# Performance work log

Measured on AMD Instinct MI355X. Metric: run time of the kernel, lower is better.

Reference implementation:

```python
import jax, jax.numpy as jnp
import numpy as np

T, B, D_IN, UNITS = 2000, 32, 512, 1024
P_KEEP = 0.8      # eval-mode dropout mask value (1 - 0.2) for 'in', 'recur', 'orig'
BN_EPS = 1e-5     # torch BatchNorm1d default eps


def setup_inputs() -> dict:
    key = jax.random.key(0)
    ks = jax.random.split(key, 6)
    s_in = 1.0 / np.sqrt(D_IN)
    s_h = 1.0 / np.sqrt(UNITS)
    # orthogonal init for recurrent mats (as in ligru_orthinit)
    uh = jnp.linalg.qr(jax.random.normal(ks[2], (UNITS, UNITS)))[0].astype(jnp.float32)
    uz = jnp.linalg.qr(jax.random.normal(ks[3], (UNITS, UNITS)))[0].astype(jnp.float32)
    return {
        "x": jax.random.normal(ks[0], (T, B, D_IN), dtype=jnp.float32),
        "Wh": jax.random.uniform(ks[1], (UNITS, D_IN), jnp.float32, -s_in, s_in),
        "Wz": jax.random.uniform(ks[4], (UNITS, D_IN), jnp.float32, -s_in, s_in),
        "Uh": uh,
        "Uz": uz,
        "gamma_wh": jnp.ones((UNITS,), jnp.float32),
        "beta_wh": jnp.zeros((UNITS,), jnp.float32),
        "gamma_wz": jnp.ones((UNITS,), jnp.float32),
        "beta_wz": jnp.zeros((UNITS,), jnp.float32),
    }


def _batchnorm(y, gamma, beta):
    # BatchNorm1d over flattened (T*B, UNITS), biased variance (training-style stats)
    yf = y.reshape(-1, y.shape[-1])
    mean = yf.mean(axis=0)
    var = yf.var(axis=0)
    return (y - mean) * jax.lax.rsqrt(var + BN_EPS) * gamma + beta


def reference(x, Wh, Wz, Uh, Uz, gamma_wh, beta_wh, gamma_wz, beta_wz):
    # input dropout (eval mode -> constant scale 0.8) then linear, no bias (BN on)
    xd = x * P_KEEP
    wh_out = _batchnorm(jnp.einsum("tbd,ud->tbu", xd, Wh), gamma_wh, beta_wh)
    wz_out = _batchnorm(jnp.einsum("tbd,ud->tbu", xd, Wz), gamma_wz, beta_wz)

    h0 = jnp.zeros((x.shape[1], Wh.shape[0]), x.dtype)

    def step(h, inp):
        whk, wzk = inp
        z = jax.nn.sigmoid(wzk + (h * P_KEEP) @ Uz.T)   # update gate
        a = whk + (h * P_KEEP) @ Uh.T                   # candidate pre-activation
        hcand = jax.nn.relu(a) * P_KEEP                 # 'orig' dropout scale
        h_new = z * h + (1.0 - z) * hcand
        return h_new, h_new

    _, hs = jax.lax.scan(step, h0, (wh_out, wz_out))    # hs: [T, B, UNITS]
    return hs
```

## Files before the change

### kernel.cpp

```cpp
#include <hip/hip_runtime.h>


#define T_STEPS 2000
#define NCOLS   2048
#define PKEEP   0.8f
#define BN_EPSF 1e-5f

typedef __attribute__((ext_vector_type(8))) short bf16x8;
typedef __attribute__((ext_vector_type(4))) float f32x4;
typedef __attribute__((ext_vector_type(4))) unsigned int u32x4;

static __device__ __forceinline__ unsigned short f2bf(float f) {
  unsigned u = __builtin_bit_cast(unsigned, f);
  unsigned r = u + 0x7FFFu + ((u >> 16) & 1u);
  return (unsigned short)(r >> 16);
}
static __device__ __forceinline__ float bf2f(unsigned short s) {
  unsigned u = ((unsigned)s) << 16;
  return __builtin_bit_cast(float, u);
}

__global__ void k_convw(const float* __restrict__ Wh, const float* __restrict__ Wz,
                        unsigned short* __restrict__ Wb) {
  int i = blockIdx.x * 256 + threadIdx.x;
  int e = i * 4;
  int n = e >> 9;
  int k = e & 511;
  const float* src = (n < 1024) ? (Wh + (size_t)n * 512 + k)
                                : (Wz + (size_t)(n - 1024) * 512 + k);
  float4 v = *(const float4*)src;
  *(ushort4*)(Wb + e) = make_ushort4(f2bf(v.x), f2bf(v.y), f2bf(v.z), f2bf(v.w));
}

__global__ __launch_bounds__(256, 2) void k_gemm(
    const float* __restrict__ X, const unsigned short* __restrict__ Wb,
    unsigned short* __restrict__ P, float* __restrict__ sums, float* __restrict__ sumsq) {
  __shared__ __align__(16) unsigned short As[128 * 32];
  __shared__ __align__(16) unsigned short Bs[128 * 32];
  const int tid  = threadIdx.x;
  const int bm   = blockIdx.x >> 4, bn = blockIdx.x & 15;
  const int lane = tid & 63, wid = tid >> 6;
  const int wm   = wid >> 1, wn = wid & 1;
  const int lrow = lane & 15, lk = lane >> 4;

  f32x4 acc[4][4] = {};

  for (int kk = 0; kk < 512; kk += 32) {
    __syncthreads();
#pragma unroll
    for (int j = 0; j < 2; ++j) {
      int c = j * 256 + wid * 64 + lane;
      int brow = c >> 2, b8 = (c & 3) * 8;
      const unsigned short* gp = Wb + (size_t)(bn * 128 + brow) * 512 + kk + b8;
      __builtin_amdgcn_global_load_lds(
          (const __attribute__((address_space(1))) unsigned int*)gp,
          (__attribute__((address_space(3))) unsigned int*)(Bs + (size_t)(j * 256 + wid * 64) * 8),
          16, 0, 0);
    }
    {
      int arow = tid >> 1, ahalf = tid & 1;
      const float4* xp = (const float4*)(X + (size_t)(bm * 128 + arow) * 512 + kk + ahalf * 16);
      unsigned v[8];
#pragma unroll
      for (int j = 0; j < 4; ++j) {
        float4 f = xp[j];
        v[j * 2 + 0] = (unsigned)f2bf(f.x) | ((unsigned)f2bf(f.y) << 16);
        v[j * 2 + 1] = (unsigned)f2bf(f.z) | ((unsigned)f2bf(f.w) << 16);
      }
      u32x4* ap = (u32x4*)(As + arow * 32 + ahalf * 16);
      u32x4 t0 = {v[0], v[1], v[2], v[3]};
      u32x4 t1 = {v[4], v[5], v[6], v[7]};
      ap[0] = t0; ap[1] = t1;
    }
    __syncthreads();

    bf16x8 af[4], bfr[4];
#pragma unroll
    for (int mt = 0; mt < 4; ++mt)
      af[mt] = *(const bf16x8*)(As + (wm * 64 + mt * 16 + lrow) * 32 + lk * 8);
#pragma unroll
    for (int nt = 0; nt < 4; ++nt)
      bfr[nt] = *(const bf16x8*)(Bs + (wn * 64 + nt * 16 + lrow) * 32 + lk * 8);
#pragma unroll
    for (int mt = 0; mt < 4; ++mt)
#pragma unroll
      for (int nt = 0; nt < 4; ++nt)
        acc[mt][nt] = __builtin_amdgcn_mfma_f32_16x16x32_bf16(af[mt], bfr[nt], acc[mt][nt], 0, 0, 0);
  }

#pragma unroll
  for (int mt = 0; mt < 4; ++mt)
#pragma unroll
    for (int nt = 0; nt < 4; ++nt) {
      f32x4 a = acc[mt][nt];
      int gcol  = bn * 128 + wn * 64 + nt * 16 + lrow;
      int grow0 = bm * 128 + wm * 64 + mt * 16 + lk * 4;
#pragma unroll
      for (int rr = 0; rr < 4; ++rr)
        P[(size_t)(grow0 + rr) * NCOLS + gcol] = f2bf(a[rr]);
    }
#pragma unroll
  for (int nt = 0; nt < 4; ++nt) {
    float s = 0.f, q = 0.f;
#pragma unroll
    for (int mt = 0; mt < 4; ++mt) {
      f32x4 a = acc[mt][nt];
#pragma unroll
      for (int rr = 0; rr < 4; ++rr) { s += a[rr]; q += a[rr] * a[rr]; }
    }
    s += __shfl_xor(s, 16); s += __shfl_xor(s, 32);
    q += __shfl_xor(q, 16); q += __shfl_xor(q, 32);
    if (lane < 16) {
      int gcol = bn * 128 + wn * 64 + nt * 16 + lrow;
      atomicAdd(&sums[gcol], s);
      atomicAdd(&sumsq[gcol], q);
    }
  }
}

__global__ __launch_bounds__(256, 1) void k_scan(
    const float* __restrict__ Uh, const float* __restrict__ Uz,
    const float* __restrict__ gwh, const float* __restrict__ bwh,
    const float* __restrict__ gwz, const float* __restrict__ bwz,
    const unsigned short* P,
    const float* __restrict__ sums, const float* __restrict__ sumsq,
    unsigned long long* hrec,
    float* out)
{
  __shared__ __align__(16) unsigned char hlds[8192];
  __shared__ __align__(16) float zlds[128];

  const int tid  = threadIdx.x;
  const int g    = blockIdx.x & 7;
  const int r    = blockIdx.x >> 3;
  const int lane = tid & 63;
  const int wid  = tid >> 6;
  const int lrow = lane & 15, lk = lane >> 4;
  const int b0   = g * 4;
  const int u0   = r * 32;
  const int uw   = u0 + (wid & 1) * 16;
  const bool isZ = (wid < 2);
  const int uu   = uw + lrow;
  const int col  = isZ ? (1024 + uu) : uu;

  float scl, bia;
  {
    float s = sums[col], q = sumsq[col];
    float gam = isZ ? gwz[uu] : gwh[uu];
    float bet = isZ ? bwz[uu] : bwh[uu];
    float mean = s * (1.0f / 64000.0f);
    float var  = q * (1.0f / 64000.0f) - mean * mean;
    float rstd = rsqrtf(var + BN_EPSF);
    scl = gam * rstd;
    bia = bet - mean * scl;
  }

  const float* urow = (isZ ? Uz : Uh) + (size_t)uu * 1024;
  bf16x8 bfrag[32];
#pragma unroll
  for (int kt = 0; kt < 32; ++kt) {
    const float4* p4 = (const float4*)(urow + kt * 32 + lk * 8);
    float4 fa = p4[0], fb = p4[1];
    bf16x8 t;
    t[0] = (short)f2bf(fa.x * PKEEP); t[1] = (short)f2bf(fa.y * PKEEP);
    t[2] = (short)f2bf(fa.z * PKEEP); t[3] = (short)f2bf(fa.w * PKEEP);
    t[4] = (short)f2bf(fb.x * PKEEP); t[5] = (short)f2bf(fb.y * PKEEP);
    t[6] = (short)f2bf(fb.z * PKEEP); t[7] = (short)f2bf(fb.w * PKEEP);
    bfrag[kt] = t;
  }

  unsigned short pf[4];
#pragma unroll
  for (int rr = 0; rr < 4; ++rr)
    pf[rr] = P[(size_t)(b0 + rr) * NCOLS + col];

  f32x4 hown = {0.f, 0.f, 0.f, 0.f};

  for (int t = 0; t < T_STEPS; ++t) {
    unsigned long long rec[8];
    {
      const unsigned long long* rb = hrec + (((size_t)(g * 2 + (t & 1))) << 11);
#pragma unroll
      for (int j = 0; j < 8; ++j)
        rec[j] = __hip_atomic_load(rb + tid + 256 * j, __ATOMIC_RELAXED, __HIP_MEMORY_SCOPE_SYSTEM);
      while (true) {
        unsigned bad = 0;
#pragma unroll
        for (int j = 0; j < 8; ++j)
          if ((unsigned)(rec[j] >> 32) < (unsigned)t) bad |= (1u << j);
        if (!bad) break;
        __builtin_amdgcn_s_sleep(1);
#pragma unroll
        for (int j = 0; j < 8; ++j)
          if (bad & (1u << j))
            rec[j] = __hip_atomic_load(rb + tid + 256 * j, __ATOMIC_RELAXED, __HIP_MEMORY_SCOPE_SYSTEM);
      }
#pragma unroll
      for (int j = 0; j < 8; ++j) {
        int idx = tid + 256 * j;
        int row = idx >> 9, up = idx & 511;
        int byteoff = (row * 2048 + up * 4) ^ ((row & 3) << 5);
        *(unsigned*)(hlds + byteoff) = (unsigned)rec[j];
      }
    }
    __syncthreads();

    unsigned short pn[4] = {pf[0], pf[1], pf[2], pf[3]};
    if (t + 1 < T_STEPS) {
#pragma unroll
      for (int rr = 0; rr < 4; ++rr)
        pn[rr] = P[(size_t)((t + 1) * 32 + b0 + rr) * NCOLS + col];
    }

    f32x4 ac0 = {0.f, 0.f, 0.f, 0.f}, ac1 = ac0, ac2 = ac0, ac3 = ac0;
#pragma unroll
    for (int kt = 0; kt < 32; ++kt) {
      int ab = (((lane & 3) * 2048) + kt * 64 + lk * 16) ^ ((lane & 3) << 5);
      bf16x8 af = *(const bf16x8*)(hlds + ab);
      if ((kt & 3) == 0)      ac0 = __builtin_amdgcn_mfma_f32_16x16x32_bf16(af, bfrag[kt], ac0, 0, 0, 0);
      else if ((kt & 3) == 1) ac1 = __builtin_amdgcn_mfma_f32_16x16x32_bf16(af, bfrag[kt], ac1, 0, 0, 0);
      else if ((kt & 3) == 2) ac2 = __builtin_amdgcn_mfma_f32_16x16x32_bf16(af, bfrag[kt], ac2, 0, 0, 0);
      else                    ac3 = __builtin_amdgcn_mfma_f32_16x16x32_bf16(af, bfrag[kt], ac3, 0, 0, 0);
    }
    f32x4 dsum = (ac0 + ac1) + (ac2 + ac3);

    float pre[4];
#pragma unroll
    for (int rr = 0; rr < 4; ++rr)
      pre[rr] = dsum[rr] + bf2f(pf[rr]) * scl + bia;

    if (isZ && lane < 16) {
      f32x4 zv;
#pragma unroll
      for (int rr = 0; rr < 4; ++rr) zv[rr] = 1.0f / (1.0f + __expf(-pre[rr]));
      *(f32x4*)(zlds + ((wid & 1) * 16 + lrow) * 4) = zv;
    }
    __syncthreads();

    if (!isZ && lane < 16) {
      f32x4 zv = *(const f32x4*)(zlds + ((wid & 1) * 16 + lrow) * 4);
      f32x4 hn;
#pragma unroll
      for (int rr = 0; rr < 4; ++rr) {
        float hc = fmaxf(pre[rr], 0.0f) * PKEEP;
        hn[rr] = zv[rr] * hown[rr] + (1.0f - zv[rr]) * hc;
      }
      hown = hn;
      float o[4];
#pragma unroll
      for (int rr = 0; rr < 4; ++rr) o[rr] = __shfl_xor(hn[rr], 1);
      if ((lane & 1) == 0) {
        unsigned long long* hbn = hrec + (((size_t)(g * 2 + ((t + 1) & 1))) << 11);
        unsigned tagw = (unsigned)(t + 1);
#pragma unroll
        for (int rr = 0; rr < 4; ++rr) {
          float2 ov = {hn[rr], o[rr]};
          *(float2*)(out + (size_t)(t * 32 + b0 + rr) * 1024 + uu) = ov;
          unsigned long long rcd = ((unsigned long long)tagw << 32)
                                 | (unsigned)f2bf(hn[rr]) | ((unsigned)f2bf(o[rr]) << 16);
          __hip_atomic_store(hbn + rr * 512 + (uu >> 1), rcd,
                             __ATOMIC_RELAXED, __HIP_MEMORY_SCOPE_SYSTEM);
        }
      }
    }

#pragma unroll
    for (int rr = 0; rr < 4; ++rr) pf[rr] = pn[rr];
  }
}

extern "C" void kernel_launch(void* const* d_in, const int* in_sizes, int n_in,
                              void* d_out, int out_size, void* d_ws, size_t ws_size,
                              hipStream_t stream) {
  (void)in_sizes; (void)n_in; (void)out_size; (void)ws_size;
  const float* x   = (const float*)d_in[0];
  const float* Wh  = (const float*)d_in[1];
  const float* Wz  = (const float*)d_in[2];
  const float* Uh  = (const float*)d_in[3];
  const float* Uz  = (const float*)d_in[4];
  const float* gwh = (const float*)d_in[5];
  const float* bwh = (const float*)d_in[6];
  const float* gwz = (const float*)d_in[7];
  const float* bwz = (const float*)d_in[8];

  char* ws = (char*)d_ws;
  float*              sums  = (float*)(ws + 0);
  float*              sumsq = (float*)(ws + 8192);
  unsigned long long* hrec  = (unsigned long long*)(ws + 16384);
  unsigned short*     Wb    = (unsigned short*)(ws + 278528);

  hipMemsetAsync(d_ws, 0, 278528, stream);
  k_convw<<<1024, 256, 0, stream>>>(Wh, Wz, Wb);
  k_gemm<<<8000, 256, 0, stream>>>(x, Wb, (unsigned short*)d_out, sums, sumsq);
  k_scan<<<256, 256, 0, stream>>>(Uh, Uz, gwh, bwh, gwz, bwz,
                                  (const unsigned short*)d_out, sums, sumsq,
                                  hrec, (float*)d_out);
}
```

Before: 7.258 ms.

## Halve scan workgroups, fuse both gates per wave, pin batch groups to XCCs

The recurrent scan kernel drops from 256 to 128 workgroups. Each wave now holds both the Uh and Uz fragments and computes both gates itself, which removes the intra-block z exchange through LDS and the second barrier. Workgroups read their XCC ID and, when the placement allows, map each batch group onto a single XCC so they can use plain volatile loads and stores for the h exchange instead of system-scope atomics. The pre-activation projections are prefetched into a triple-buffered LDS ring with global_load_lds. The costs are doubled register pressure and reliance on a grid-wide spin barrier at startup, which assumes all 128 workgroups are resident at once.

```diff
diff --git a/kernel.cpp b/kernel.cpp
--- a/kernel.cpp
+++ b/kernel.cpp
@@ -5,6 +5,8 @@
 #define NCOLS   2048
 #define PKEEP   0.8f
 #define BN_EPSF 1e-5f
+#define NW      128
+#define WPG     16
 
 typedef __attribute__((ext_vector_type(8))) short bf16x8;
 typedef __attribute__((ext_vector_type(4))) float f32x4;
@@ -125,147 +127,211 @@
     const unsigned short* P,
     const float* __restrict__ sums, const float* __restrict__ sumsq,
     unsigned long long* hrec,
+    unsigned int* ctrl,
     float* out)
 {
   __shared__ __align__(16) unsigned char hlds[8192];
-  __shared__ __align__(16) float zlds[128];
+  __shared__ __align__(16) unsigned char plds[3072];
+  __shared__ int sgrp[3];
 
   const int tid  = threadIdx.x;
-  const int g    = blockIdx.x & 7;
-  const int r    = blockIdx.x >> 3;
   const int lane = tid & 63;
   const int wid  = tid >> 6;
   const int lrow = lane & 15, lk = lane >> 4;
-  const int b0   = g * 4;
-  const int u0   = r * 32;
-  const int uw   = u0 + (wid & 1) * 16;
-  const bool isZ = (wid < 2);
-  const int uu   = uw + lrow;
-  const int col  = isZ ? (1024 + uu) : uu;
-
-  float scl, bia;
+
+  if (tid == 0) {
+    unsigned xcc;
+    asm volatile("s_getreg_b32 %0, hwreg(HW_REG_XCC_ID)" : "=s"(xcc));
+    xcc &= 15u;
+    unsigned idx = atomicAdd(&ctrl[xcc], 1u);
+    __hip_atomic_fetch_add(&ctrl[16], 1u, __ATOMIC_RELEASE, __HIP_MEMORY_SCOPE_SYSTEM);
+    while (__hip_atomic_load(&ctrl[16], __ATOMIC_RELAXED, __HIP_MEMORY_SCOPE_SYSTEM) < NW)
+      __builtin_amdgcn_s_sleep(8);
+    __builtin_amdgcn_fence(__ATOMIC_ACQUIRE, "agent");
+    bool reg = (xcc < 8u) && (idx < WPG);
+    if (reg)
+      for (int i = 0; i < 8; ++i)
+        reg = reg && (__hip_atomic_load(&ctrl[i], __ATOMIC_RELAXED,
+                                        __HIP_MEMORY_SCOPE_SYSTEM) == WPG);
+    if (reg) {
+      sgrp[0] = (int)xcc; sgrp[1] = (int)idx; sgrp[2] = 1;
+    } else {
+      unsigned rank = atomicAdd(&ctrl[17], 1u);
+      sgrp[0] = (int)(rank & 7u); sgrp[1] = (int)(rank >> 3); sgrp[2] = 0;
+    }
+  }
+  __syncthreads();
+  const int  g     = sgrp[0];
+  const int  role  = sgrp[1];
+  const bool fastp = (sgrp[2] != 0);
+  const int  b0    = g * 4;
+  const int  wu    = wid * 16 + lrow;
+  const int  uu    = role * 64 + wu;
+
+  float sclh, biah, sclz, biaz;
   {
-    float s = sums[col], q = sumsq[col];
-    float gam = isZ ? gwz[uu] : gwh[uu];
-    float bet = isZ ? bwz[uu] : bwh[uu];
+    float s = sums[uu], q = sumsq[uu];
     float mean = s * (1.0f / 64000.0f);
     float var  = q * (1.0f / 64000.0f) - mean * mean;
     float rstd = rsqrtf(var + BN_EPSF);
-    scl = gam * rstd;
-    bia = bet - mean * scl;
-  }
-
-  const float* urow = (isZ ? Uz : Uh) + (size_t)uu * 1024;
-  bf16x8 bfrag[32];
-#pragma unroll
-  for (int kt = 0; kt < 32; ++kt) {
-    const float4* p4 = (const float4*)(urow + kt * 32 + lk * 8);
-    float4 fa = p4[0], fb = p4[1];
-    bf16x8 t;
-    t[0] = (short)f2bf(fa.x * PKEEP); t[1] = (short)f2bf(fa.y * PKEEP);
-    t[2] = (short)f2bf(fa.z * PKEEP); t[3] = (short)f2bf(fa.w * PKEEP);
-    t[4] = (short)f2bf(fb.x * PKEEP); t[5] = (short)f2bf(fb.y * PKEEP);
-    t[6] = (short)f2bf(fb.z * PKEEP); t[7] = (short)f2bf(fb.w * PKEEP);
-    bfrag[kt] = t;
-  }
-
-  unsigned short pf[4];
-#pragma unroll
-  for (int rr = 0; rr < 4; ++rr)
-    pf[rr] = P[(size_t)(b0 + rr) * NCOLS + col];
+    sclh = gwh[uu] * rstd; biah = bwh[uu] - mean * sclh;
+    s = sums[1024 + uu]; q = sumsq[1024 + uu];
+    mean = s * (1.0f / 64000.0f);
+    var  = q * (1.0f / 64000.0f) - mean * mean;
+    rstd = rsqrtf(var + BN_EPSF);
+    sclz = gwz[uu] * rstd; biaz = bwz[uu] - mean * sclz;
+  }
+
+  bf16x8 bh[32], bz[32];
+  {
+    const float* uhrow = Uh + (size_t)uu * 1024;
+    const float* uzrow = Uz + (size_t)uu * 1024;
+#pragma unroll
+    for (int kt = 0; kt < 32; ++kt) {
+      const float4* p4 = (const float4*)(uhrow + kt * 32 + lk * 8);
+      float4 fa = p4[0], fb = p4[1];
+      bf16x8 tv;
+      tv[0] = (short)f2bf(fa.x * PKEEP); tv[1] = (short)f2bf(fa.y * PKEEP);
+      tv[2] = (short)f2bf(fa.z * PKEEP); tv[3] = (short)f2bf(fa.w * PKEEP);
+      tv[4] = (short)f2bf(fb.x * PKEEP); tv[5] = (short)f2bf(fb.y * PKEEP);
+      tv[6] = (short)f2bf(fb.z * PKEEP); tv[7] = (short)f2bf(fb.w * PKEEP);
+      bh[kt] = tv;
+      const float4* q4 = (const float4*)(uzrow + kt * 32 + lk * 8);
+      fa = q4[0]; fb = q4[1];
+      tv[0] = (short)f2bf(fa.x * PKEEP); tv[1] = (short)f2bf(fa.y * PKEEP);
+      tv[2] = (short)f2bf(fa.z * PKEEP); tv[3] = (short)f2bf(fa.w * PKEEP);
+      tv[4] = (short)f2bf(fb.x * PKEEP); tv[5] = (short)f2bf(fb.y * PKEEP);
+      tv[6] = (short)f2bf(fb.z * PKEEP); tv[7] = (short)f2bf(fb.w * PKEEP);
+      bz[kt] = tv;
+    }
+  }
+
+  if (wid == 0) {
+#pragma unroll
+    for (int tt = 0; tt < 2; ++tt) {
+      int seg = lane >> 3, sub = lane & 7;
+      int rr = seg & 3, gate = seg >> 2;
+      const unsigned short* src = P + (size_t)(tt * 32 + b0 + rr) * NCOLS
+                                  + gate * 1024 + role * 64 + sub * 8;
+      __builtin_amdgcn_global_load_lds(
+          (const __attribute__((address_space(1))) unsigned int*)src,
+          (__attribute__((address_space(3))) unsigned int*)(plds + tt * 1024),
+          16, 0, 0);
+    }
+  }
+  __syncthreads();
+
+  if (tid == 0) {
+    __hip_atomic_fetch_add(&ctrl[18], 1u, __ATOMIC_RELEASE, __HIP_MEMORY_SCOPE_SYSTEM);
+    while (__hip_atomic_load(&ctrl[18], __ATOMIC_RELAXED, __HIP_MEMORY_SCOPE_SYSTEM) < NW)
+      __builtin_amdgcn_s_sleep(8);
+  }
+  __syncthreads();
 
   f32x4 hown = {0.f, 0.f, 0.f, 0.f};
+  int cur = 0;
 
   for (int t = 0; t < T_STEPS; ++t) {
+    const unsigned long long* rb = hrec + (((size_t)(g * 2 + (t & 1))) << 11);
     unsigned long long rec[8];
+#pragma unroll
+    for (int j = 0; j < 8; ++j)
+      rec[j] = fastp ? *(volatile const unsigned long long*)(rb + tid + 256 * j)
+                     : __hip_atomic_load(rb + tid + 256 * j, __ATOMIC_RELAXED,
+                                         __HIP_MEMORY_SCOPE_SYSTEM);
+    while (true) {
+      unsigned bad = 0;
+#pragma unroll
+      for (int j = 0; j < 8; ++j)
+        if ((unsigned)(rec[j] >> 32) < (unsigned)t) bad |= (1u << j);
+      if (__ballot(bad != 0) == 0ull) break;
+      __builtin_amdgcn_s_sleep(1);
+#pragma unroll
+      for (int j = 0; j < 8; ++j)
+        if (bad & (1u << j))
+          rec[j] = fastp ? *(volatile const unsigned long long*)(rb + tid + 256 * j)
+                         : __hip_atomic_load(rb + tid + 256 * j, __ATOMIC_RELAXED,
+                                             __HIP_MEMORY_SCOPE_SYSTEM);
+    }
+
+    if (wid == 0 && t + 2 < T_STEPS) {
+      int nx2 = cur + 2; if (nx2 >= 3) nx2 -= 3;
+      int seg = lane >> 3, sub = lane & 7;
+      int rr = seg & 3, gate = seg >> 2;
+      const unsigned short* src = P + (size_t)((t + 2) * 32 + b0 + rr) * NCOLS
+                                  + gate * 1024 + role * 64 + sub * 8;
+      __builtin_amdgcn_global_load_lds(
+          (const __attribute__((address_space(1))) unsigned int*)src,
+          (__attribute__((address_space(3))) unsigned int*)(plds + nx2 * 1024),
+          16, 0, 0);
+    }
+
+#pragma unroll
+    for (int j = 0; j < 8; ++j) {
+      int idx = tid + 256 * j;
+      int row = idx >> 9, up = idx & 511;
+      int byteoff = (row * 2048 + up * 4) ^ ((row & 3) << 5);
+      *(unsigned*)(hlds + byteoff) = (unsigned)rec[j];
+    }
+    asm volatile("s_waitcnt lgkmcnt(0)" ::: "memory");
+    __builtin_amdgcn_sched_barrier(0);
+    __builtin_amdgcn_s_barrier();
+    asm volatile("" ::: "memory");
+
+    f32x4 ah0 = {0.f, 0.f, 0.f, 0.f}, ah1 = ah0, az0 = ah0, az1 = ah0;
+#pragma unroll
+    for (int kt = 0; kt < 32; ++kt) {
+      int ab = ((lane & 3) * 2048 + kt * 64 + lk * 16) ^ ((lane & 3) << 5);
+      bf16x8 af = *(const bf16x8*)(hlds + ab);
+      if (kt & 1) {
+        az1 = __builtin_amdgcn_mfma_f32_16x16x32_bf16(af, bz[kt], az1, 0, 0, 0);
+        ah1 = __builtin_amdgcn_mfma_f32_16x16x32_bf16(af, bh[kt], ah1, 0, 0, 0);
+      } else {
+        az0 = __builtin_amdgcn_mfma_f32_16x16x32_bf16(af, bz[kt], az0, 0, 0, 0);
+        ah0 = __builtin_amdgcn_mfma_f32_16x16x32_bf16(af, bh[kt], ah0, 0, 0, 0);
+      }
+    }
+
+    const unsigned short* pl = (const unsigned short*)(plds + cur * 1024);
+    float hn4[4], on4[4];
     {
-      const unsigned long long* rb = hrec + (((size_t)(g * 2 + (t & 1))) << 11);
-#pragma unroll
-      for (int j = 0; j < 8; ++j)
-        rec[j] = __hip_atomic_load(rb + tid + 256 * j, __ATOMIC_RELAXED, __HIP_MEMORY_SCOPE_SYSTEM);
-      while (true) {
-        unsigned bad = 0;
-#pragma unroll
-        for (int j = 0; j < 8; ++j)
-          if ((unsigned)(rec[j] >> 32) < (unsigned)t) bad |= (1u << j);
-        if (!bad) break;
-        __builtin_amdgcn_s_sleep(1);
-#pragma unroll
-        for (int j = 0; j < 8; ++j)
-          if (bad & (1u << j))
-            rec[j] = __hip_atomic_load(rb + tid + 256 * j, __ATOMIC_RELAXED, __HIP_MEMORY_SCOPE_SYSTEM);
-      }
-#pragma unroll
-      for (int j = 0; j < 8; ++j) {
-        int idx = tid + 256 * j;
-        int row = idx >> 9, up = idx & 511;
-        int byteoff = (row * 2048 + up * 4) ^ ((row & 3) << 5);
-        *(unsigned*)(hlds + byteoff) = (unsigned)rec[j];
-      }
-    }
-    __syncthreads();
-
-    unsigned short pn[4] = {pf[0], pf[1], pf[2], pf[3]};
-    if (t + 1 < T_STEPS) {
-#pragma unroll
-      for (int rr = 0; rr < 4; ++rr)
-        pn[rr] = P[(size_t)((t + 1) * 32 + b0 + rr) * NCOLS + col];
-    }
-
-    f32x4 ac0 = {0.f, 0.f, 0.f, 0.f}, ac1 = ac0, ac2 = ac0, ac3 = ac0;
-#pragma unroll
-    for (int kt = 0; kt < 32; ++kt) {
-      int ab = (((lane & 3) * 2048) + kt * 64 + lk * 16) ^ ((lane & 3) << 5);
-      bf16x8 af = *(const bf16x8*)(hlds + ab);
-      if ((kt & 3) == 0)      ac0 = __builtin_amdgcn_mfma_f32_16x16x32_bf16(af, bfrag[kt], ac0, 0, 0, 0);
-      else if ((kt & 3) == 1) ac1 = __builtin_amdgcn_mfma_f32_16x16x32_bf16(af, bfrag[kt], ac1, 0, 0, 0);
-      else if ((kt & 3) == 2) ac2 = __builtin_amdgcn_mfma_f32_16x16x32_bf16(af, bfrag[kt], ac2, 0, 0, 0);
-      else                    ac3 = __builtin_amdgcn_mfma_f32_16x16x32_bf16(af, bfrag[kt], ac3, 0, 0, 0);
-    }
-    f32x4 dsum = (ac0 + ac1) + (ac2 + ac3);
-
-    float pre[4];
-#pragma unroll
-    for (int rr = 0; rr < 4; ++rr)
-      pre[rr] = dsum[rr] + bf2f(pf[rr]) * scl + bia;
-
-    if (isZ && lane < 16) {
-      f32x4 zv;
-#pragma unroll
-      for (int rr = 0; rr < 4; ++rr) zv[rr] = 1.0f / (1.0f + __expf(-pre[rr]));
-      *(f32x4*)(zlds + ((wid & 1) * 16 + lrow) * 4) = zv;
-    }
-    __syncthreads();
-
-    if (!isZ && lane < 16) {
-      f32x4 zv = *(const f32x4*)(zlds + ((wid & 1) * 16 + lrow) * 4);
-      f32x4 hn;
+      f32x4 dh = ah0 + ah1, dz = az0 + az1;
 #pragma unroll
       for (int rr = 0; rr < 4; ++rr) {
-        float hc = fmaxf(pre[rr], 0.0f) * PKEEP;
-        hn[rr] = zv[rr] * hown[rr] + (1.0f - zv[rr]) * hc;
-      }
-      hown = hn;
-      float o[4];
-#pragma unroll
-      for (int rr = 0; rr < 4; ++rr) o[rr] = __shfl_xor(hn[rr], 1);
-      if ((lane & 1) == 0) {
-        unsigned long long* hbn = hrec + (((size_t)(g * 2 + ((t + 1) & 1))) << 11);
-        unsigned tagw = (unsigned)(t + 1);
-#pragma unroll
-        for (int rr = 0; rr < 4; ++rr) {
-          float2 ov = {hn[rr], o[rr]};
-          *(float2*)(out + (size_t)(t * 32 + b0 + rr) * 1024 + uu) = ov;
-          unsigned long long rcd = ((unsigned long long)tagw << 32)
-                                 | (unsigned)f2bf(hn[rr]) | ((unsigned)f2bf(o[rr]) << 16);
+        float prh = dh[rr] + bf2f(pl[rr * 64 + wu]) * sclh + biah;
+        float prz = dz[rr] + bf2f(pl[(4 + rr) * 64 + wu]) * sclz + biaz;
+        float zz = 1.0f / (1.0f + __expf(-prz));
+        float hc = fmaxf(prh, 0.0f) * PKEEP;
+        float hv = zz * hown[rr] + (1.0f - zz) * hc;
+        hown[rr] = hv;
+        hn4[rr] = hv;
+      }
+    }
+#pragma unroll
+    for (int rr = 0; rr < 4; ++rr) on4[rr] = __shfl_xor(hn4[rr], 1);
+
+    asm volatile("s_waitcnt vmcnt(1)" ::: "memory");
+
+    if (lane < 16 && (lane & 1) == 0) {
+      unsigned long long* hbn = hrec + (((size_t)(g * 2 + ((t + 1) & 1))) << 11);
+      unsigned tagw = (unsigned)(t + 1);
+#pragma unroll
+      for (int rr = 0; rr < 4; ++rr) {
+        unsigned long long rcd = ((unsigned long long)tagw << 32)
+                               | (unsigned)f2bf(hn4[rr]) | ((unsigned)f2bf(on4[rr]) << 16);
+        if (fastp)
+          *(volatile unsigned long long*)(hbn + rr * 512 + (uu >> 1)) = rcd;
+        else
           __hip_atomic_store(hbn + rr * 512 + (uu >> 1), rcd,
                              __ATOMIC_RELAXED, __HIP_MEMORY_SCOPE_SYSTEM);
-        }
-      }
-    }
-
-#pragma unroll
-    for (int rr = 0; rr < 4; ++rr) pf[rr] = pn[rr];
+      }
+#pragma unroll
+      for (int rr = 0; rr < 4; ++rr) {
+        float2 ov = {hn4[rr], on4[rr]};
+        *(float2*)(out + (size_t)(t * 32 + b0 + rr) * 1024 + uu) = ov;
+      }
+    }
+    cur = cur + 1; if (cur >= 3) cur = 0;
   }
 }
 
@@ -287,12 +353,13 @@
   float*              sums  = (float*)(ws + 0);
   float*              sumsq = (float*)(ws + 8192);
   unsigned long long* hrec  = (unsigned long long*)(ws + 16384);
-  unsigned short*     Wb    = (unsigned short*)(ws + 278528);
-
-  hipMemsetAsync(d_ws, 0, 278528, stream);
+  unsigned int*       ctrl  = (unsigned int*)(ws + 278528);
+  unsigned short*     Wb    = (unsigned short*)(ws + 278784);
+
+  hipMemsetAsync(d_ws, 0, 278784, stream);
   k_convw<<<1024, 256, 0, stream>>>(Wh, Wz, Wb);
   k_gemm<<<8000, 256, 0, stream>>>(x, Wb, (unsigned short*)d_out, sums, sumsq);
-  k_scan<<<256, 256, 0, stream>>>(Uh, Uz, gwh, bwh, gwz, bwz,
-                                  (const unsigned short*)d_out, sums, sumsq,
-                                  hrec, (float*)d_out);
-}
+  k_scan<<<NW, 256, 0, stream>>>(Uh, Uz, gwh, bwh, gwz, bwz,
+                                 (const unsigned short*)d_out, sums, sumsq,
+                                 hrec, ctrl, (float*)d_out);
+}
```

Measured after the change: 11.00 ms. 51.5% more time.

## Interleave z/h gates per wave and drop second block barrier in scan

Applied to the files above, without the earlier changes.

Each wave in the scan kernel now computes both gates for 8 units: lanes 0-7 hold the z gate and lanes 8-15 the h gate, and the z preactivation reaches the h lanes through a lane shuffle. This removes the shared-memory z exchange and the second __syncthreads per timestep. The h buffer in LDS is double-buffered so one barrier per step is enough, the P prefetch runs two steps ahead, and a startup grid barrier makes all blocks wait until every block is resident. The costs are an extra spin on a global counter at launch and manual waitcnt and scheduling barriers that need careful ordering.

```diff
diff --git a/kernel.cpp b/kernel.cpp
--- a/kernel.cpp
+++ b/kernel.cpp
@@ -5,6 +5,7 @@
 #define NCOLS   2048
 #define PKEEP   0.8f
 #define BN_EPSF 1e-5f
+#define NW      256
 
 typedef __attribute__((ext_vector_type(8))) short bf16x8;
 typedef __attribute__((ext_vector_type(4))) float f32x4;
@@ -125,29 +126,29 @@
     const unsigned short* P,
     const float* __restrict__ sums, const float* __restrict__ sumsq,
     unsigned long long* hrec,
+    unsigned int* ctrl,
     float* out)
 {
-  __shared__ __align__(16) unsigned char hlds[8192];
-  __shared__ __align__(16) float zlds[128];
+  __shared__ __align__(16) unsigned char hlds[16384];
 
   const int tid  = threadIdx.x;
-  const int g    = blockIdx.x & 7;
-  const int r    = blockIdx.x >> 3;
   const int lane = tid & 63;
   const int wid  = tid >> 6;
   const int lrow = lane & 15, lk = lane >> 4;
+
+  const int g    = blockIdx.x & 7;
+  const int role = blockIdx.x >> 3;
   const int b0   = g * 4;
-  const int u0   = r * 32;
-  const int uw   = u0 + (wid & 1) * 16;
-  const bool isZ = (wid < 2);
-  const int uu   = uw + lrow;
-  const int col  = isZ ? (1024 + uu) : uu;
+  const int u0w  = role * 32 + wid * 8;
+  const bool isH = (lrow >= 8);
+  const int unit = u0w + (lrow & 7);
+  const int col  = isH ? unit : (1024 + unit);
 
   float scl, bia;
   {
     float s = sums[col], q = sumsq[col];
-    float gam = isZ ? gwz[uu] : gwh[uu];
-    float bet = isZ ? bwz[uu] : bwh[uu];
+    float gam = isH ? gwh[unit] : gwz[unit];
+    float bet = isH ? bwh[unit] : bwz[unit];
     float mean = s * (1.0f / 64000.0f);
     float var  = q * (1.0f / 64000.0f) - mean * mean;
     float rstd = rsqrtf(var + BN_EPSF);
@@ -155,68 +156,84 @@
     bia = bet - mean * scl;
   }
 
-  const float* urow = (isZ ? Uz : Uh) + (size_t)uu * 1024;
+  const float* urow = (isH ? Uh : Uz) + (size_t)unit * 1024;
   bf16x8 bfrag[32];
 #pragma unroll
   for (int kt = 0; kt < 32; ++kt) {
     const float4* p4 = (const float4*)(urow + kt * 32 + lk * 8);
     float4 fa = p4[0], fb = p4[1];
-    bf16x8 t;
-    t[0] = (short)f2bf(fa.x * PKEEP); t[1] = (short)f2bf(fa.y * PKEEP);
-    t[2] = (short)f2bf(fa.z * PKEEP); t[3] = (short)f2bf(fa.w * PKEEP);
-    t[4] = (short)f2bf(fb.x * PKEEP); t[5] = (short)f2bf(fb.y * PKEEP);
-    t[6] = (short)f2bf(fb.z * PKEEP); t[7] = (short)f2bf(fb.w * PKEEP);
-    bfrag[kt] = t;
-  }
-
-  unsigned short pf[4];
-#pragma unroll
-  for (int rr = 0; rr < 4; ++rr)
-    pf[rr] = P[(size_t)(b0 + rr) * NCOLS + col];
+    bf16x8 tv;
+    tv[0] = (short)f2bf(fa.x * PKEEP); tv[1] = (short)f2bf(fa.y * PKEEP);
+    tv[2] = (short)f2bf(fa.z * PKEEP); tv[3] = (short)f2bf(fa.w * PKEEP);
+    tv[4] = (short)f2bf(fb.x * PKEEP); tv[5] = (short)f2bf(fb.y * PKEEP);
+    tv[6] = (short)f2bf(fb.z * PKEEP); tv[7] = (short)f2bf(fb.w * PKEEP);
+    bfrag[kt] = tv;
+  }
+
+  unsigned short pf[4], pn1[4];
+#pragma unroll
+  for (int rr = 0; rr < 4; ++rr) {
+    pf[rr]  = P[(size_t)(b0 + rr) * NCOLS + col];
+    pn1[rr] = P[(size_t)(32 + b0 + rr) * NCOLS + col];
+  }
+  __syncthreads();
+
+  if (tid == 0) {
+    __hip_atomic_fetch_add(&ctrl[0], 1u, __ATOMIC_RELEASE, __HIP_MEMORY_SCOPE_SYSTEM);
+    while (__hip_atomic_load(&ctrl[0], __ATOMIC_RELAXED, __HIP_MEMORY_SCOPE_SYSTEM) < NW)
+      __builtin_amdgcn_s_sleep(8);
+  }
+  __syncthreads();
 
   f32x4 hown = {0.f, 0.f, 0.f, 0.f};
 
   for (int t = 0; t < T_STEPS; ++t) {
+    const int par = t & 1;
+
+    const unsigned long long* rb = hrec + (((size_t)(g * 2 + par)) << 11) + tid;
     unsigned long long rec[8];
-    {
-      const unsigned long long* rb = hrec + (((size_t)(g * 2 + (t & 1))) << 11);
+#pragma unroll
+    for (int j = 0; j < 8; ++j)
+      rec[j] = __hip_atomic_load(rb + 256 * j, __ATOMIC_RELAXED, __HIP_MEMORY_SCOPE_SYSTEM);
+    while (true) {
+      unsigned bad = 0;
 #pragma unroll
       for (int j = 0; j < 8; ++j)
-        rec[j] = __hip_atomic_load(rb + tid + 256 * j, __ATOMIC_RELAXED, __HIP_MEMORY_SCOPE_SYSTEM);
-      while (true) {
-        unsigned bad = 0;
-#pragma unroll
-        for (int j = 0; j < 8; ++j)
-          if ((unsigned)(rec[j] >> 32) < (unsigned)t) bad |= (1u << j);
-        if (!bad) break;
-        __builtin_amdgcn_s_sleep(1);
-#pragma unroll
-        for (int j = 0; j < 8; ++j)
-          if (bad & (1u << j))
-            rec[j] = __hip_atomic_load(rb + tid + 256 * j, __ATOMIC_RELAXED, __HIP_MEMORY_SCOPE_SYSTEM);
-      }
-#pragma unroll
-      for (int j = 0; j < 8; ++j) {
-        int idx = tid + 256 * j;
-        int row = idx >> 9, up = idx & 511;
-        int byteoff = (row * 2048 + up * 4) ^ ((row & 3) << 5);
-        *(unsigned*)(hlds + byteoff) = (unsigned)rec[j];
-      }
-    }
-    __syncthreads();
-
-    unsigned short pn[4] = {pf[0], pf[1], pf[2], pf[3]};
-    if (t + 1 < T_STEPS) {
+        if ((unsigned)(rec[j] >> 32) < (unsigned)t) bad |= (1u << j);
+      if (!bad) break;
+      __builtin_amdgcn_s_sleep(1);
+#pragma unroll
+      for (int j = 0; j < 8; ++j)
+        if (bad & (1u << j))
+          rec[j] = __hip_atomic_load(rb + 256 * j, __ATOMIC_RELAXED, __HIP_MEMORY_SCOPE_SYSTEM);
+    }
+    asm volatile("s_waitcnt vmcnt(0)" ::: "memory");
+
+    unsigned short pn2[4] = {0, 0, 0, 0};
+    if (t + 2 < T_STEPS) {
 #pragma unroll
       for (int rr = 0; rr < 4; ++rr)
-        pn[rr] = P[(size_t)((t + 1) * 32 + b0 + rr) * NCOLS + col];
-    }
+        pn2[rr] = P[(size_t)((t + 2) * 32 + b0 + rr) * NCOLS + col];
+    }
+
+    unsigned char* hb = hlds + par * 8192;
+#pragma unroll
+    for (int j = 0; j < 8; ++j) {
+      int idx = tid + 256 * j;
+      int row = idx >> 9, up = idx & 511;
+      int byteoff = (row * 2048 + up * 4) ^ ((row & 3) << 5);
+      *(unsigned*)(hb + byteoff) = (unsigned)rec[j];
+    }
+    asm volatile("s_waitcnt lgkmcnt(0)" ::: "memory");
+    __builtin_amdgcn_sched_barrier(0);
+    __builtin_amdgcn_s_barrier();
+    __builtin_amdgcn_sched_barrier(0);
 
     f32x4 ac0 = {0.f, 0.f, 0.f, 0.f}, ac1 = ac0, ac2 = ac0, ac3 = ac0;
 #pragma unroll
     for (int kt = 0; kt < 32; ++kt) {
-      int ab = (((lane & 3) * 2048) + kt * 64 + lk * 16) ^ ((lane & 3) << 5);
-      bf16x8 af = *(const bf16x8*)(hlds + ab);
+      int ab = ((lane & 3) * 2048 + kt * 64 + lk * 16) ^ ((lane & 3) << 5);
+      bf16x8 af = *(const bf16x8*)(hb + ab);
       if ((kt & 3) == 0)      ac0 = __builtin_amdgcn_mfma_f32_16x16x32_bf16(af, bfrag[kt], ac0, 0, 0, 0);
       else if ((kt & 3) == 1) ac1 = __builtin_amdgcn_mfma_f32_16x16x32_bf16(af, bfrag[kt], ac1, 0, 0, 0);
       else if ((kt & 3) == 2) ac2 = __builtin_amdgcn_mfma_f32_16x16x32_bf16(af, bfrag[kt], ac2, 0, 0, 0);
@@ -224,48 +241,46 @@
     }
     f32x4 dsum = (ac0 + ac1) + (ac2 + ac3);
 
-    float pre[4];
-#pragma unroll
-    for (int rr = 0; rr < 4; ++rr)
+    float pre[4], oth[4];
+#pragma unroll
+    for (int rr = 0; rr < 4; ++rr) {
       pre[rr] = dsum[rr] + bf2f(pf[rr]) * scl + bia;
-
-    if (isZ && lane < 16) {
-      f32x4 zv;
-#pragma unroll
-      for (int rr = 0; rr < 4; ++rr) zv[rr] = 1.0f / (1.0f + __expf(-pre[rr]));
-      *(f32x4*)(zlds + ((wid & 1) * 16 + lrow) * 4) = zv;
-    }
-    __syncthreads();
-
-    if (!isZ && lane < 16) {
-      f32x4 zv = *(const f32x4*)(zlds + ((wid & 1) * 16 + lrow) * 4);
-      f32x4 hn;
+      oth[rr] = __shfl_xor(pre[rr], 8);
+    }
+
+    if (lk == 0 && isH) {
+      float hn[4];
 #pragma unroll
       for (int rr = 0; rr < 4; ++rr) {
+        float zz = 1.0f / (1.0f + __expf(-oth[rr]));
         float hc = fmaxf(pre[rr], 0.0f) * PKEEP;
-        hn[rr] = zv[rr] * hown[rr] + (1.0f - zv[rr]) * hc;
+        hn[rr] = zz * hown[rr] + (1.0f - zz) * hc;
+        hown[rr] = hn[rr];
       }
-      hown = hn;
-      float o[4];
-#pragma unroll
-      for (int rr = 0; rr < 4; ++rr) o[rr] = __shfl_xor(hn[rr], 1);
+      float pp[4];
+#pragma unroll
+      for (int rr = 0; rr < 4; ++rr) pp[rr] = __shfl_xor(hn[rr], 1);
       if ((lane & 1) == 0) {
-        unsigned long long* hbn = hrec + (((size_t)(g * 2 + ((t + 1) & 1))) << 11);
+        unsigned long long* hbn = hrec + (((size_t)(g * 2 + ((t + 1) & 1))) << 11)
+                                + (unit >> 1);
         unsigned tagw = (unsigned)(t + 1);
 #pragma unroll
         for (int rr = 0; rr < 4; ++rr) {
-          float2 ov = {hn[rr], o[rr]};
-          *(float2*)(out + (size_t)(t * 32 + b0 + rr) * 1024 + uu) = ov;
           unsigned long long rcd = ((unsigned long long)tagw << 32)
-                                 | (unsigned)f2bf(hn[rr]) | ((unsigned)f2bf(o[rr]) << 16);
-          __hip_atomic_store(hbn + rr * 512 + (uu >> 1), rcd,
+                                 | (unsigned)f2bf(hn[rr]) | ((unsigned)f2bf(pp[rr]) << 16);
+          __hip_atomic_store(hbn + rr * 512, rcd,
                              __ATOMIC_RELAXED, __HIP_MEMORY_SCOPE_SYSTEM);
         }
+#pragma unroll
+        for (int rr = 0; rr < 4; ++rr) {
+          float2 ov = {hn[rr], pp[rr]};
+          *(float2*)(out + (size_t)(t * 32 + b0 + rr) * 1024 + unit) = ov;
+        }
       }
     }
 
 #pragma unroll
-    for (int rr = 0; rr < 4; ++rr) pf[rr] = pn[rr];
+    for (int rr = 0; rr < 4; ++rr) { pf[rr] = pn1[rr]; pn1[rr] = pn2[rr]; }
   }
 }
 
@@ -287,12 +302,13 @@
   float*              sums  = (float*)(ws + 0);
   float*              sumsq = (float*)(ws + 8192);
   unsigned long long* hrec  = (unsigned long long*)(ws + 16384);
-  unsigned short*     Wb    = (unsigned short*)(ws + 278528);
-
-  hipMemsetAsync(d_ws, 0, 278528, stream);
+  unsigned int*       ctrl  = (unsigned int*)(ws + 278528);
+  unsigned short*     Wb    = (unsigned short*)(ws + 278784);
+
+  hipMemsetAsync(d_ws, 0, 278784, stream);
   k_convw<<<1024, 256, 0, stream>>>(Wh, Wz, Wb);
   k_gemm<<<8000, 256, 0, stream>>>(x, Wb, (unsigned short*)d_out, sums, sumsq);
-  k_scan<<<256, 256, 0, stream>>>(Uh, Uz, gwh, bwh, gwz, bwz,
-                                  (const unsigned short*)d_out, sums, sumsq,
-                                  hrec, (float*)d_out);
-}
+  k_scan<<<NW, 256, 0, stream>>>(Uh, Uz, gwh, bwh, gwz, bwz,
+                                 (const unsigned short*)d_out, sums, sumsq,
+                                 hrec, ctrl, (float*)d_out);
+}
```

After: 7.818 ms. 7.7% more time.
